# Kernel optimization log

Measured on AMD Instinct MI355X. Metric: run time of the kernel, lower is better.

The kernel has to match this reference:

```python
import jax, jax.numpy as jnp
import numpy as np

B, S, E, H = 2, 2048, 512, 8
D = E // H  # head_dim = 64


def setup_inputs() -> dict:
    key = jax.random.key(0)
    ks = jax.random.split(key, 10)
    sc = 1.0 / np.sqrt(E)
    x = jax.random.normal(ks[0], (B, S, E), dtype=jnp.float32)
    # parent index per node: tree_structure[b][parent[b,i]] contains i
    parent = jax.random.randint(ks[1], (B, S), 0, S, dtype=jnp.int32)
    Wp = jax.random.normal(ks[2], (E, E), dtype=jnp.float32) * sc
    bp = jnp.zeros((E,), dtype=jnp.float32)
    Wc = jax.random.normal(ks[3], (E, E), dtype=jnp.float32) * sc
    bc = jnp.zeros((E,), dtype=jnp.float32)
    Ws = jax.random.normal(ks[4], (E, E), dtype=jnp.float32) * sc
    bs = jnp.zeros((E,), dtype=jnp.float32)
    Wo = jax.random.normal(ks[5], (E, E), dtype=jnp.float32) * sc
    bo = jnp.zeros((E,), dtype=jnp.float32)
    return {"x": x, "parent": parent, "Wp": Wp, "bp": bp, "Wc": Wc,
            "bc": bc, "Ws": Ws, "bs": bs, "Wo": Wo, "bo": bo}


def _tree_mask(parent):
    # Vectorized equivalent of the per-batch scatter loop:
    # mask[b, p, c] = mask[b, c, p] = 1 for each (parent, child) edge.
    b_idx = jnp.arange(B)[:, None]
    rows = jnp.arange(S)[None, :]
    m = jnp.zeros((B, S, S), dtype=bool)
    m = m.at[b_idx, rows, parent].set(True)
    m = m.at[b_idx, parent, rows].set(True)
    return m  # (B, S, S), broadcast over heads


def reference(x, parent, Wp, bp, Wc, bc, Ws, bs, Wo, bo):
    # Tri-projection
    p = (x @ Wp + bp).reshape(B, S, H, D)
    c = (x @ Wc + bc).reshape(B, S, H, D)
    s = (x @ Ws + bs).reshape(B, S, H, D)
    scores = jnp.einsum('bnhd,bmhd->bnhm', p, c) / jnp.sqrt(jnp.float32(D))
    mask = _tree_mask(parent)  # (B, S, S)
    scores = jnp.where(mask[:, :, None, :], scores, -jnp.inf)
    attn = jax.nn.softmax(scores, axis=-1)  # dropout is identity (train=False)
    out = jnp.einsum('bnhm,bmhd->bnhd', attn, s).reshape(B, S, E)
    return out @ Wo + bo
```

## Files before the change

kernel.cpp:

```cpp
#include <hip/hip_runtime.h>
#include <hip/hip_bf16.h>

#define B_  2
#define S_  2048
#define E_  512
#define H_  8
#define D_  64
#define BS_ (B_ * S_)
#define N1_ 1536
#define K_  512

typedef __bf16 bf16x8 __attribute__((ext_vector_type(8)));
typedef float  f32x4  __attribute__((ext_vector_type(4)));

__device__ __forceinline__ ushort f2bf(float f) {
    unsigned u = __float_as_uint(f);
    unsigned r = (u + 0x7FFFu + ((u >> 16) & 1u)) >> 16;
    return (ushort)r;
}

__device__ __forceinline__ void gld_lds16(const ushort* g, ushort* l) {
    __builtin_amdgcn_global_load_lds(
        (const __attribute__((address_space(1))) unsigned int*)g,
        (__attribute__((address_space(3))) unsigned int*)l, 16, 0, 0);
}


__global__ void convert_x_kernel(const float* __restrict__ x,
                                 ushort* __restrict__ xb, int n4) {
    int i = blockIdx.x * blockDim.x + threadIdx.x;
    if (i >= n4) return;
    float4 v = ((const float4*)x)[i];
    ushort4 o;
    o.x = f2bf(v.x); o.y = f2bf(v.y); o.z = f2bf(v.z); o.w = f2bf(v.w);
    ((ushort4*)xb)[i] = o;
}

__global__ __launch_bounds__(256) void transpose_all_kernel(
    const float* __restrict__ Wp, const float* __restrict__ Wc,
    const float* __restrict__ Ws, const float* __restrict__ Wo,
    ushort* __restrict__ Wcat_t, ushort* __restrict__ Wo_t) {
    __shared__ ushort T[64][65];
    int z = blockIdx.z;
    const float* src = (z == 0) ? Wp : (z == 1) ? Wc : (z == 2) ? Ws : Wo;
    ushort* dst = (z < 3) ? (Wcat_t + (size_t)z * 512 * 512) : Wo_t;
    int n0 = blockIdx.x * 64, k0 = blockIdx.y * 64;
    int tid = threadIdx.x;
    int g = tid >> 6, l = tid & 63;
    #pragma unroll
    for (int r = 0; r < 16; r++) {
        int kk = g * 16 + r;
        T[kk][l] = f2bf(src[(size_t)(k0 + kk) * 512 + n0 + l]);
    }
    __syncthreads();
    #pragma unroll
    for (int r = 0; r < 16; r++) {
        int nn = g * 16 + r;
        dst[(size_t)(n0 + nn) * 512 + k0 + l] = T[l][nn];
    }
}

template<int TN>
__global__ __launch_bounds__(256) void gemm_mfma_kernel(
    const ushort* __restrict__ A,
    const ushort* __restrict__ Bt,
    const float*  __restrict__ b0,
    const float*  __restrict__ b1,
    const float*  __restrict__ b2,
    float* __restrict__ C,
    int N, int K) {
    constexpr int TM = 128, TK = 64;
    constexpr int NF = TN / 32;
    __shared__ ushort As[TM][TK];
    __shared__ ushort Bs[TN][TK];

    const int tid  = threadIdx.x;
    const int lane = tid & 63;
    const int wave = tid >> 6;
    const int wm = wave >> 1, wn = wave & 1;
    const int row0 = blockIdx.y * TM;
    const int col0 = blockIdx.x * TN;

    f32x4 acc[4][NF] = {};

    const int srow = lane >> 3;
    const int scol = (lane & 7) * 8;

    const int lrow = lane & 15;
    const int lk   = (lane >> 4) * 8;

    for (int kt = 0; kt < K; kt += TK) {
        const ushort* ga = A + (size_t)(row0 + wave * 32 + srow) * K + kt + scol;
        #pragma unroll
        for (int j = 0; j < 4; j++)
            gld_lds16(ga + (size_t)j * 8 * K, &As[wave * 32 + j * 8][0]);
        const ushort* gb = Bt + (size_t)(col0 + wave * (TN / 4) + srow) * K + kt + scol;
        #pragma unroll
        for (int j = 0; j < NF; j++)
            gld_lds16(gb + (size_t)j * 8 * K, &Bs[wave * (TN / 4) + j * 8][0]);
        __syncthreads();

        #pragma unroll
        for (int kk = 0; kk < TK; kk += 32) {
            bf16x8 af[4], bf[NF];
            #pragma unroll
            for (int i = 0; i < 4; i++)
                af[i] = *(const bf16x8*)(&As[wm * 64 + i * 16 + lrow][kk + lk]);
            #pragma unroll
            for (int j = 0; j < NF; j++)
                bf[j] = *(const bf16x8*)(&Bs[wn * (TN / 2) + j * 16 + lrow][kk + lk]);
            #pragma unroll
            for (int i = 0; i < 4; i++)
                #pragma unroll
                for (int j = 0; j < NF; j++)
                    acc[i][j] = __builtin_amdgcn_mfma_f32_16x16x32_bf16(
                        af[i], bf[j], acc[i][j], 0, 0, 0);
        }
        __syncthreads();
    }

    const int ccol = lane & 15;
    const int crow = (lane >> 4) * 4;
    #pragma unroll
    for (int j = 0; j < NF; j++) {
        int gcol = col0 + wn * (TN / 2) + j * 16 + ccol;
        float bias = (gcol < 512) ? b0[gcol]
                   : (gcol < 1024) ? b1[gcol - 512] : b2[gcol - 1024];
        #pragma unroll
        for (int i = 0; i < 4; i++) {
            int grow = row0 + wm * 64 + i * 16 + crow;
            #pragma unroll
            for (int rg = 0; rg < 4; rg++)
                C[(size_t)(grow + rg) * N + gcol] = acc[i][j][rg] + bias;
        }
    }
}

__global__ __launch_bounds__(256) void tree_attn_kernel(
    const float* __restrict__ PCS, const int* __restrict__ parent,
    float* __restrict__ Z, float* __restrict__ acc) {
    int gtid = blockIdx.x * blockDim.x + threadIdx.x;
    int w    = gtid >> 6;
    int lane = gtid & 63;
    int b = w >> 11;
    int i = w & (S_ - 1);
    int par = parent[w];
    int rp  = (b << 11) + par;
    bool dup = (parent[rp] == i);

    const float* rowN = PCS + (size_t)w  * N1_;
    const float* rowM = PCS + (size_t)rp * N1_;

    for (int h = 0; h < H_; h++) {
        int o = h * 64 + lane;
        float pn = rowN[o];
        float cm = rowM[512 + o];
        float sm = rowM[1024 + o];
        float sc = pn * cm;
        #pragma unroll
        for (int off = 32; off; off >>= 1) sc += __shfl_xor(sc, off);
        float e = expf(sc * 0.125f);
        atomicAdd(&acc[(size_t)w * E_ + o], e * sm);
        if (lane == 0) atomicAdd(&Z[w * H_ + h], e);

        if (!dup) {
            float pm = rowM[o];
            float cn = rowN[512 + o];
            float sn = rowN[1024 + o];
            float sc2 = pm * cn;
            #pragma unroll
            for (int off = 32; off; off >>= 1) sc2 += __shfl_xor(sc2, off);
            float e2 = expf(sc2 * 0.125f);
            atomicAdd(&acc[(size_t)rp * E_ + o], e2 * sn);
            if (lane == 0) atomicAdd(&Z[rp * H_ + h], e2);
        }
    }
}

__global__ void normalize_kernel(const float* __restrict__ acc,
                                 const float* __restrict__ Z,
                                 ushort* __restrict__ attn) {
    int i = blockIdx.x * blockDim.x + threadIdx.x;
    attn[i] = f2bf(acc[i] / Z[i >> 6]);
}

extern "C" void kernel_launch(void* const* d_in, const int* in_sizes, int n_in,
                              void* d_out, int out_size, void* d_ws, size_t ws_size,
                              hipStream_t stream) {
    const float* x      = (const float*)d_in[0];
    const int*   parent = (const int*)  d_in[1];
    const float* Wp     = (const float*)d_in[2];
    const float* bp     = (const float*)d_in[3];
    const float* Wc     = (const float*)d_in[4];
    const float* bc     = (const float*)d_in[5];
    const float* Ws     = (const float*)d_in[6];
    const float* bs     = (const float*)d_in[7];
    const float* Wo     = (const float*)d_in[8];
    const float* bo     = (const float*)d_in[9];
    float* out = (float*)d_out;

    char* ws = (char*)d_ws;
    ushort* x_bf    = (ushort*)(ws + 0);
    ushort* Wcat_t  = (ushort*)(ws + 4194304);
    ushort* Wo_t    = (ushort*)(ws + 5767168);
    float*  PCS     = (float*) (ws + 6291456);
    float*  Zd      = (float*) (ws + 31457280);
    float*  accd    = (float*) (ws + 31588352);
    ushort* attn_bf = (ushort*)(ws + 39976960);

    hipMemsetAsync(Zd,   0, (size_t)BS_ * H_ * sizeof(float), stream);
    hipMemsetAsync(accd, 0, (size_t)BS_ * E_ * sizeof(float), stream);

    convert_x_kernel<<<(BS_ * E_ / 4 + 255) / 256, 256, 0, stream>>>(
        x, x_bf, BS_ * E_ / 4);
    transpose_all_kernel<<<dim3(8, 8, 4), 256, 0, stream>>>(
        Wp, Wc, Ws, Wo, Wcat_t, Wo_t);

    gemm_mfma_kernel<128><<<dim3(N1_ / 128, BS_ / 128), 256, 0, stream>>>(
        x_bf, Wcat_t, bp, bc, bs, PCS, N1_, K_);

    tree_attn_kernel<<<BS_ * 64 / 256, 256, 0, stream>>>(PCS, parent, Zd, accd);
    normalize_kernel<<<BS_ * E_ / 256, 256, 0, stream>>>(accd, Zd, attn_bf);

    gemm_mfma_kernel<64><<<dim3(E_ / 64, BS_ / 128), 256, 0, stream>>>(
        attn_bf, Wo_t, bo, bo, bo, out, E_, K_);
}
```

Before: 141.0 us.

## Replace atomic scatter tree attention with per-node gather and bf16 projections

Tree attention moves from a scatter scheme to a gather scheme. Before, each node did float atomicAdds into its own and its parent's accumulators, then a separate normalize kernel ran. Now each wave owns one node, scores its parent edge, then finds its children by ballot-scanning the whole parent array. It keeps per-head softmax sums in registers and writes normalized bf16 output directly, which removes the memsets, the atomics and the normalize kernel. The projection GEMM also writes bf16 instead of fp32 to halve intermediate traffic. The trade-off is that every wave scans all 2048 parent entries of its batch, and the intermediates lose precision.

```diff
diff --git a/kernel.cpp b/kernel.cpp
--- a/kernel.cpp
+++ b/kernel.cpp
@@ -17,6 +17,15 @@
     unsigned u = __float_as_uint(f);
     unsigned r = (u + 0x7FFFu + ((u >> 16) & 1u)) >> 16;
     return (ushort)r;
+}
+__device__ __forceinline__ float bf2f(ushort b) {
+    return __uint_as_float(((unsigned)b) << 16);
+}
+
+__device__ __forceinline__ float wave_sum(float v) {
+    #pragma unroll
+    for (int off = 32; off; off >>= 1) v += __shfl_xor(v, off);
+    return v;
 }
 
 __device__ __forceinline__ void gld_lds16(const ushort* g, ushort* l) {
@@ -60,14 +69,14 @@
     }
 }
 
-template<int TN>
+template<int TN, bool BF16OUT>
 __global__ __launch_bounds__(256) void gemm_mfma_kernel(
     const ushort* __restrict__ A,
     const ushort* __restrict__ Bt,
     const float*  __restrict__ b0,
     const float*  __restrict__ b1,
     const float*  __restrict__ b2,
-    float* __restrict__ C,
+    void* __restrict__ Cv,
     int N, int K) {
     constexpr int TM = 128, TK = 64;
     constexpr int NF = TN / 32;
@@ -102,19 +111,19 @@
 
         #pragma unroll
         for (int kk = 0; kk < TK; kk += 32) {
-            bf16x8 af[4], bf[NF];
+            bf16x8 af[4], bfr[NF];
             #pragma unroll
             for (int i = 0; i < 4; i++)
                 af[i] = *(const bf16x8*)(&As[wm * 64 + i * 16 + lrow][kk + lk]);
             #pragma unroll
             for (int j = 0; j < NF; j++)
-                bf[j] = *(const bf16x8*)(&Bs[wn * (TN / 2) + j * 16 + lrow][kk + lk]);
+                bfr[j] = *(const bf16x8*)(&Bs[wn * (TN / 2) + j * 16 + lrow][kk + lk]);
             #pragma unroll
             for (int i = 0; i < 4; i++)
                 #pragma unroll
                 for (int j = 0; j < NF; j++)
                     acc[i][j] = __builtin_amdgcn_mfma_f32_16x16x32_bf16(
-                        af[i], bf[j], acc[i][j], 0, 0, 0);
+                        af[i], bfr[j], acc[i][j], 0, 0, 0);
         }
         __syncthreads();
     }
@@ -130,58 +139,69 @@
         for (int i = 0; i < 4; i++) {
             int grow = row0 + wm * 64 + i * 16 + crow;
             #pragma unroll
-            for (int rg = 0; rg < 4; rg++)
-                C[(size_t)(grow + rg) * N + gcol] = acc[i][j][rg] + bias;
-        }
-    }
-}
-
-__global__ __launch_bounds__(256) void tree_attn_kernel(
-    const float* __restrict__ PCS, const int* __restrict__ parent,
-    float* __restrict__ Z, float* __restrict__ acc) {
+            for (int rg = 0; rg < 4; rg++) {
+                float v = acc[i][j][rg] + bias;
+                if (BF16OUT)
+                    ((ushort*)Cv)[(size_t)(grow + rg) * N + gcol] = f2bf(v);
+                else
+                    ((float*)Cv)[(size_t)(grow + rg) * N + gcol] = v;
+            }
+        }
+    }
+}
+
+__global__ __launch_bounds__(256) void attn_gather_kernel(
+    const ushort* __restrict__ PCS, const int* __restrict__ parent,
+    ushort* __restrict__ attn) {
     int gtid = blockIdx.x * blockDim.x + threadIdx.x;
     int w    = gtid >> 6;
     int lane = gtid & 63;
-    int b = w >> 11;
-    int i = w & (S_ - 1);
-    int par = parent[w];
-    int rp  = (b << 11) + par;
-    bool dup = (parent[rp] == i);
-
-    const float* rowN = PCS + (size_t)w  * N1_;
-    const float* rowM = PCS + (size_t)rp * N1_;
-
-    for (int h = 0; h < H_; h++) {
-        int o = h * 64 + lane;
-        float pn = rowN[o];
-        float cm = rowM[512 + o];
-        float sm = rowM[1024 + o];
-        float sc = pn * cm;
-        #pragma unroll
-        for (int off = 32; off; off >>= 1) sc += __shfl_xor(sc, off);
-        float e = expf(sc * 0.125f);
-        atomicAdd(&acc[(size_t)w * E_ + o], e * sm);
-        if (lane == 0) atomicAdd(&Z[w * H_ + h], e);
-
-        if (!dup) {
-            float pm = rowM[o];
-            float cn = rowN[512 + o];
-            float sn = rowN[1024 + o];
-            float sc2 = pm * cn;
-            #pragma unroll
-            for (int off = 32; off; off >>= 1) sc2 += __shfl_xor(sc2, off);
-            float e2 = expf(sc2 * 0.125f);
-            atomicAdd(&acc[(size_t)rp * E_ + o], e2 * sn);
-            if (lane == 0) atomicAdd(&Z[rp * H_ + h], e2);
-        }
-    }
-}
-
-__global__ void normalize_kernel(const float* __restrict__ acc,
-                                 const float* __restrict__ Z,
-                                 ushort* __restrict__ attn) {
-    int i = blockIdx.x * blockDim.x + threadIdx.x;
-    attn[i] = f2bf(acc[i] / Z[i >> 6]);
+    int bbase = ((w >> 11) << 11);
+    int i  = w & (S_ - 1);
+    int rp = bbase + parent[w];
+
+    float pn[H_];
+    #pragma unroll
+    for (int h = 0; h < H_; h++)
+        pn[h] = bf2f(PCS[(size_t)w * N1_ + h * 64 + lane]);
+
+    float Zh[H_], avh[H_];
+    {
+        const ushort* rm = PCS + (size_t)rp * N1_;
+        #pragma unroll
+        for (int h = 0; h < H_; h++) {
+            float cm = bf2f(rm[512 + h * 64 + lane]);
+            float sm = bf2f(rm[1024 + h * 64 + lane]);
+            float sc = wave_sum(pn[h] * cm);
+            float e = __expf(sc * 0.125f);
+            Zh[h]  = e;
+            avh[h] = e * sm;
+        }
+    }
+
+    for (int t0 = 0; t0 < S_; t0 += 64) {
+        int m = bbase + t0 + lane;
+        unsigned long long mask = __ballot(parent[m] == i);
+        while (mask) {
+            int l = __ffsll(mask) - 1;
+            mask &= mask - 1;
+            int c = bbase + t0 + l;
+            if (c == rp) continue;
+            const ushort* rc = PCS + (size_t)c * N1_;
+            #pragma unroll
+            for (int h = 0; h < H_; h++) {
+                float cc = bf2f(rc[512 + h * 64 + lane]);
+                float sc = wave_sum(pn[h] * cc);
+                float e = __expf(sc * 0.125f);
+                Zh[h]  += e;
+                avh[h] += e * bf2f(rc[1024 + h * 64 + lane]);
+            }
+        }
+    }
+
+    #pragma unroll
+    for (int h = 0; h < H_; h++)
+        attn[(size_t)w * E_ + h * 64 + lane] = f2bf(avh[h] / Zh[h]);
 }
 
 extern "C" void kernel_launch(void* const* d_in, const int* in_sizes, int n_in,
@@ -203,25 +223,20 @@
     ushort* x_bf    = (ushort*)(ws + 0);
     ushort* Wcat_t  = (ushort*)(ws + 4194304);
     ushort* Wo_t    = (ushort*)(ws + 5767168);
-    float*  PCS     = (float*) (ws + 6291456);
-    float*  Zd      = (float*) (ws + 31457280);
-    float*  accd    = (float*) (ws + 31588352);
-    ushort* attn_bf = (ushort*)(ws + 39976960);
-
-    hipMemsetAsync(Zd,   0, (size_t)BS_ * H_ * sizeof(float), stream);
-    hipMemsetAsync(accd, 0, (size_t)BS_ * E_ * sizeof(float), stream);
+    ushort* PCS_bf  = (ushort*)(ws + 6291456);
+    ushort* attn_bf = (ushort*)(ws + 18874368);
 
     convert_x_kernel<<<(BS_ * E_ / 4 + 255) / 256, 256, 0, stream>>>(
         x, x_bf, BS_ * E_ / 4);
     transpose_all_kernel<<<dim3(8, 8, 4), 256, 0, stream>>>(
         Wp, Wc, Ws, Wo, Wcat_t, Wo_t);
 
-    gemm_mfma_kernel<128><<<dim3(N1_ / 128, BS_ / 128), 256, 0, stream>>>(
-        x_bf, Wcat_t, bp, bc, bs, PCS, N1_, K_);
-
-    tree_attn_kernel<<<BS_ * 64 / 256, 256, 0, stream>>>(PCS, parent, Zd, accd);
-    normalize_kernel<<<BS_ * E_ / 256, 256, 0, stream>>>(accd, Zd, attn_bf);
-
-    gemm_mfma_kernel<64><<<dim3(E_ / 64, BS_ / 128), 256, 0, stream>>>(
+    gemm_mfma_kernel<128, true><<<dim3(N1_ / 128, BS_ / 128), 256, 0, stream>>>(
+        x_bf, Wcat_t, bp, bc, bs, PCS_bf, N1_, K_);
+
+    attn_gather_kernel<<<BS_ * 64 / 256, 256, 0, stream>>>(
+        PCS_bf, parent, attn_bf);
+
+    gemm_mfma_kernel<64, false><<<dim3(E_ / 64, BS_ / 128), 256, 0, stream>>>(
         attn_bf, Wo_t, bo, bo, bo, out, E_, K_);
 }
```

Result: faster. 125.3 us (-11.1%).
